# Kernel tuning notes

Hardware: AMD Instinct MI355X
Metric: run time of the kernel (lower is better)

The kernel has to match this reference:

```python
import jax, jax.numpy as jnp
import numpy as np

EPS = 1e-5   # BatchNorm eps (torch default)
K_IMP = 600  # hard-coded k in PointNet.forward


def _bn3(x, g, b, m, v):
    # inference-mode BatchNorm1d over [B, C, N]
    inv = g / jnp.sqrt(v + EPS)
    return (x - m[None, :, None]) * inv[None, :, None] + b[None, :, None]


def _bn2(x, g, b, m, v):
    # inference-mode BatchNorm1d over [B, C]
    inv = g / jnp.sqrt(v + EPS)
    return (x - m[None, :]) * inv[None, :] + b[None, :]


def _full(x, W1, g1, b1, m1, v1, W2, g2, b2, m2, v2, W3, g3, b3, m3, v3,
          W4, g4, b4, m4, v4, W5, g5, b5, m5, v5, L1w, g6, b6, m6, v6, L2w, L2b):
    # pointwise conv1d (k=1) == per-point matmul
    h = jax.nn.relu(_bn3(jnp.einsum('oc,bcn->bon', W1, x), g1, b1, m1, v1))
    h = jax.nn.relu(_bn3(jnp.einsum('oc,bcn->bon', W2, h), g2, b2, m2, v2))
    h = jax.nn.relu(_bn3(jnp.einsum('oc,bcn->bon', W3, h), g3, b3, m3, v3))
    h = jax.nn.relu(_bn3(jnp.einsum('oc,bcn->bon', W4, h), g4, b4, m4, v4))
    feats = jax.nn.relu(_bn3(jnp.einsum('oc,bcn->bon', W5, h), g5, b5, m5, v5))  # [B, emb, N]
    pooled = jnp.max(feats, axis=-1)                       # adaptive_max_pool1d(.,1).squeeze()
    h = jax.nn.relu(_bn2(pooled @ L1w.T, g6, b6, m6, v6))  # dropout is identity in eval
    logits = h @ L2w.T + L2b
    return logits, feats


def reference(x, W1, g1, b1, m1, v1, W2, g2, b2, m2, v2, W3, g3, b3, m3, v3,
              W4, g4, b4, m4, v4, W5, g5, b5, m5, v5, L1w, g6, b6, m6, v6, L2w, L2b):
    P = (W1, g1, b1, m1, v1, W2, g2, b2, m2, v2, W3, g3, b3, m3, v3,
         W4, g4, b4, m4, v4, W5, g5, b5, m5, v5, L1w, g6, b6, m6, v6, L2w, L2b)
    # --- extract_importance: inner model call at full N ---
    _, feats = _full(x, *P)
    B, _, N = x.shape
    imp = jnp.argmax(feats, axis=-1)  # [B, emb] point index maximizing each channel (first-occurrence, matches torch)
    # batched bincount(imp[b], minlength=N) -> [B, N]
    counts = jnp.zeros((B, N), jnp.int32).at[jnp.arange(B)[:, None], imp].add(1)
    idx = jnp.argsort(counts, axis=-1)[:, :K_IMP]          # ascending, take k least-hit bins
    x_sel = jnp.take_along_axis(x, idx[:, None, :], axis=-1)  # gather [B, 3, k]
    # --- main pass on reduced cloud ---
    logits, _ = _full(x_sel, *P)
    return logits


def setup_inputs() -> dict:
    key = jax.random.key(0)
    ks = iter(jax.random.split(key, 64))
    B, N, EMB, NCLS = 16, 8192, 1024, 40

    def randn(shape, s=1.0):
        return jax.random.normal(next(ks), shape, jnp.float32) * s

    inp = {"x": randn((B, 3, N))}
    dims = [(64, 3), (64, 64), (64, 64), (128, 64), (EMB, 128)]
    for i, (o, c) in enumerate(dims, 1):
        inp[f"W{i}"] = randn((o, c), 1.0 / np.sqrt(c))
        inp[f"g{i}"] = 1.0 + randn((o,), 0.1)
        inp[f"b{i}"] = randn((o,), 0.1)
        inp[f"m{i}"] = randn((o,), 0.1)
        inp[f"v{i}"] = jax.random.uniform(next(ks), (o,), jnp.float32, 0.5, 1.5)
    inp["L1w"] = randn((512, EMB), 1.0 / np.sqrt(EMB))
    inp["g6"] = 1.0 + randn((512,), 0.1)
    inp["b6"] = randn((512,), 0.1)
    inp["m6"] = randn((512,), 0.1)
    inp["v6"] = jax.random.uniform(next(ks), (512,), jnp.float32, 0.5, 1.5)
    inp["L2w"] = randn((NCLS, 512), 1.0 / np.sqrt(512))
    inp["L2b"] = randn((NCLS,), 0.01)
    return inp
```

## Files before the change

kernel.cpp:

```cpp
#include <hip/hip_runtime.h>
#include <cstdint>

typedef uint16_t u16;
typedef unsigned int u32;
typedef __attribute__((ext_vector_type(8))) short bf16x8;
typedef __attribute__((ext_vector_type(4))) float f32x4;

union U4V { uint4 u; bf16x8 v; };

#define EPSBN 1e-5f

__device__ __forceinline__ float bf2f(u16 h) {
  return __uint_as_float(((unsigned)h) << 16);
}
__device__ __forceinline__ u16 f2bf(float f) {
  unsigned u = __float_as_uint(f);
  unsigned r = u + 0x7fffu + ((u >> 16) & 1u);
  return (u16)(r >> 16);
}

__global__ void k0_prep(const float* __restrict__ W5,
                        const float* __restrict__ W1, const float* __restrict__ W2,
                        const float* __restrict__ W3, const float* __restrict__ W4,
                        const float* g1, const float* b1, const float* m1, const float* v1,
                        const float* g2, const float* b2, const float* m2, const float* v2,
                        const float* g3, const float* b3, const float* m3, const float* v3,
                        const float* g4, const float* b4, const float* m4, const float* v4,
                        u16* __restrict__ W5h, u16* __restrict__ W5l,
                        u16* __restrict__ W2h, u16* __restrict__ W2l,
                        u16* __restrict__ W3h, u16* __restrict__ W3l,
                        u16* __restrict__ W4h, u16* __restrict__ W4l,
                        float* __restrict__ Wf)
{
  int idx = blockIdx.x * 256 + threadIdx.x;
  if (idx < 131072) {
    int f = idx;
    int j = f & 7, l15 = (f >> 3) & 15, quad = (f >> 7) & 3, ks = (f >> 9) & 3, g = f >> 11;
    float w = W5[(g * 16 + l15) * 128 + ks * 32 + quad * 8 + j];
    u16 hi = f2bf(w);
    W5h[f] = hi;
    W5l[f] = f2bf(w - bf2f(hi));
    return;
  }
  int j = idx - 131072;
  if (j < 16384) {
    const float* src; u16 *dh, *dl; int f;
    if (j < 4096)      { src = W2; dh = W2h; dl = W2l; f = j; }
    else if (j < 8192) { src = W3; dh = W3h; dl = W3l; f = j - 4096; }
    else               { src = W4; dh = W4h; dl = W4l; f = j - 8192; }
    int jj = f & 7;
    int lane = (f >> 3) & 63;
    int t = f >> 9;
    int ks = t & 1, tn = t >> 1;
    int l15 = lane & 15, quad = lane >> 4;
    float w = src[(tn * 16 + l15) * 64 + ks * 32 + quad * 8 + jj];
    u16 hi = f2bf(w);
    dh[f] = hi;
    dl[f] = f2bf(w - bf2f(hi));
  } else if (j < 16576) {
    Wf[j] = W1[j - 16384];
  } else if (j < 16896) {
    int t = j - 16576;
    const float *g, *bb, *mm, *vv; int ch;
    if (t < 64)       { g = g1; bb = b1; mm = m1; vv = v1; ch = t;       }
    else if (t < 128) { g = g2; bb = b2; mm = m2; vv = v2; ch = t - 64;  }
    else if (t < 192) { g = g3; bb = b3; mm = m3; vv = v3; ch = t - 128; }
    else              { g = g4; bb = b4; mm = m4; vv = v4; ch = t - 192; }
    float s = g[ch] / sqrtf(vv[ch] + EPSBN);
    Wf[16576 + t] = s;
    Wf[16896 + t] = bb[ch] - mm[ch] * s;
  }
}

__global__ __launch_bounds__(128, 2) void k1_conv(
    const float* __restrict__ x, const float* __restrict__ Wf,
    const u16* __restrict__ W2h, const u16* __restrict__ W2l,
    const u16* __restrict__ W3h, const u16* __restrict__ W3l,
    const u16* __restrict__ W4h, const u16* __restrict__ W4l,
    u16* __restrict__ H4a, u16* __restrict__ H4b)
{
  __shared__ u32 T[2][64 * 68];
  __shared__ float P1[832];
  const int tid = threadIdx.x;
  const int w = tid >> 6, lane = tid & 63;
  const int l15 = lane & 15, quad = lane >> 4;
  const int base = blockIdx.x * 128 + w * 64;
  const int b = base >> 13, n0 = base & 8191;

  for (int i = tid; i < 832; i += 128)
    P1[i] = (i < 192) ? Wf[16384 + i]
          : (i < 512) ? Wf[16576 + (i - 192)]
                      : Wf[16896 + (i - 512)];
  __syncthreads();
  u32* Tw = &T[w][0];
  const float* SCs = &P1[192];
  const float* SHs = &P1[512];
  const f32x4 vzero = {0.f, 0.f, 0.f, 0.f};

  float xl0 = x[(b * 3 + 0) * 8192 + n0 + lane];
  float xl1 = x[(b * 3 + 1) * 8192 + n0 + lane];
  float xl2 = x[(b * 3 + 2) * 8192 + n0 + lane];
  float xs0[4], xs1[4], xs2[4];
  #pragma unroll
  for (int tm = 0; tm < 4; ++tm) {
    xs0[tm] = __shfl(xl0, tm * 16 + l15, 64);
    xs1[tm] = __shfl(xl1, tm * 16 + l15, 64);
    xs2[tm] = __shfl(xl2, tm * 16 + l15, 64);
  }
  bf16x8 ah[2][4], al[2][4];
  #pragma unroll
  for (int ks = 0; ks < 2; ++ks)
    #pragma unroll
    for (int tm = 0; tm < 4; ++tm) {
      u32 hp[4], lp[4];
      #pragma unroll
      for (int jp = 0; jp < 4; ++jp) {
        u32 hpair = 0, lpair = 0;
        #pragma unroll
        for (int e = 0; e < 2; ++e) {
          int ch = ks * 32 + quad * 8 + jp * 2 + e;
          float c = P1[ch * 3] * xs0[tm];
          c = fmaf(P1[ch * 3 + 1], xs1[tm], c);
          c = fmaf(P1[ch * 3 + 2], xs2[tm], c);
          float v = fmaxf(0.f, fmaf(c, SCs[ch], SHs[ch]));
          u16 hi = f2bf(v); float er = v - bf2f(hi); u16 lo = f2bf(er);
          hpair |= ((u32)hi) << (16 * e);
          lpair |= ((u32)lo) << (16 * e);
        }
        hp[jp] = hpair; lp[jp] = lpair;
      }
      U4V th, tl;
      th.u.x = hp[0]; th.u.y = hp[1]; th.u.z = hp[2]; th.u.w = hp[3];
      tl.u.x = lp[0]; tl.u.y = lp[1]; tl.u.z = lp[2]; tl.u.w = lp[3];
      ah[ks][tm] = th.v; al[ks][tm] = tl.v;
    }

  {
    f32x4 acc[4][4];
    #pragma unroll
    for (int tm = 0; tm < 4; ++tm)
      #pragma unroll
      for (int tn = 0; tn < 4; ++tn) acc[tm][tn] = vzero;
    #pragma unroll
    for (int ks = 0; ks < 2; ++ks) {
      bf16x8 bh[4], bl[4];
      #pragma unroll
      for (int tn = 0; tn < 4; ++tn) {
        int idx = ((tn * 2 + ks) * 64 + lane) * 8;
        bh[tn] = *(const bf16x8*)&W2h[idx];
        bl[tn] = *(const bf16x8*)&W2l[idx];
      }
      #pragma unroll
      for (int tm = 0; tm < 4; ++tm)
        #pragma unroll
        for (int tn = 0; tn < 4; ++tn) {
          acc[tm][tn] = __builtin_amdgcn_mfma_f32_16x16x32_bf16(ah[ks][tm], bh[tn], acc[tm][tn], 0, 0, 0);
          acc[tm][tn] = __builtin_amdgcn_mfma_f32_16x16x32_bf16(ah[ks][tm], bl[tn], acc[tm][tn], 0, 0, 0);
          acc[tm][tn] = __builtin_amdgcn_mfma_f32_16x16x32_bf16(al[ks][tm], bh[tn], acc[tm][tn], 0, 0, 0);
        }
    }
    #pragma unroll
    for (int tn = 0; tn < 4; ++tn) {
      int ch = tn * 16 + l15;
      float sc = SCs[64 + ch], sh = SHs[64 + ch];
      #pragma unroll
      for (int tm = 0; tm < 4; ++tm)
        #pragma unroll
        for (int r = 0; r < 4; ++r) {
          float v = fmaxf(0.f, fmaf(acc[tm][tn][r], sc, sh));
          u16 hi = f2bf(v); float er = v - bf2f(hi); u16 lo = f2bf(er);
          Tw[(tm * 16 + quad * 4 + r) * 68 + ch] = (u32)hi | ((u32)lo << 16);
        }
    }
  }

  #pragma unroll
  for (int ks = 0; ks < 2; ++ks)
    #pragma unroll
    for (int tm = 0; tm < 4; ++tm) {
      const uint4 p0 = *(const uint4*)&Tw[(tm * 16 + l15) * 68 + ks * 32 + quad * 8];
      const uint4 p1 = *(const uint4*)&Tw[(tm * 16 + l15) * 68 + ks * 32 + quad * 8 + 4];
      U4V th, tl;
      th.u.x = (p0.x & 0xffffu) | (p0.y << 16);
      th.u.y = (p0.z & 0xffffu) | (p0.w << 16);
      th.u.z = (p1.x & 0xffffu) | (p1.y << 16);
      th.u.w = (p1.z & 0xffffu) | (p1.w << 16);
      tl.u.x = (p0.x >> 16) | (p0.y & 0xffff0000u);
      tl.u.y = (p0.z >> 16) | (p0.w & 0xffff0000u);
      tl.u.z = (p1.x >> 16) | (p1.y & 0xffff0000u);
      tl.u.w = (p1.z >> 16) | (p1.w & 0xffff0000u);
      ah[ks][tm] = th.v; al[ks][tm] = tl.v;
    }
  {
    f32x4 acc[4][4];
    #pragma unroll
    for (int tm = 0; tm < 4; ++tm)
      #pragma unroll
      for (int tn = 0; tn < 4; ++tn) acc[tm][tn] = vzero;
    #pragma unroll
    for (int ks = 0; ks < 2; ++ks) {
      bf16x8 bh[4], bl[4];
      #pragma unroll
      for (int tn = 0; tn < 4; ++tn) {
        int idx = ((tn * 2 + ks) * 64 + lane) * 8;
        bh[tn] = *(const bf16x8*)&W3h[idx];
        bl[tn] = *(const bf16x8*)&W3l[idx];
      }
      #pragma unroll
      for (int tm = 0; tm < 4; ++tm)
        #pragma unroll
        for (int tn = 0; tn < 4; ++tn) {
          acc[tm][tn] = __builtin_amdgcn_mfma_f32_16x16x32_bf16(ah[ks][tm], bh[tn], acc[tm][tn], 0, 0, 0);
          acc[tm][tn] = __builtin_amdgcn_mfma_f32_16x16x32_bf16(ah[ks][tm], bl[tn], acc[tm][tn], 0, 0, 0);
          acc[tm][tn] = __builtin_amdgcn_mfma_f32_16x16x32_bf16(al[ks][tm], bh[tn], acc[tm][tn], 0, 0, 0);
        }
    }
    #pragma unroll
    for (int tn = 0; tn < 4; ++tn) {
      int ch = tn * 16 + l15;
      float sc = SCs[128 + ch], sh = SHs[128 + ch];
      #pragma unroll
      for (int tm = 0; tm < 4; ++tm)
        #pragma unroll
        for (int r = 0; r < 4; ++r) {
          float v = fmaxf(0.f, fmaf(acc[tm][tn][r], sc, sh));
          u16 hi = f2bf(v); float er = v - bf2f(hi); u16 lo = f2bf(er);
          Tw[(tm * 16 + quad * 4 + r) * 68 + ch] = (u32)hi | ((u32)lo << 16);
        }
    }
  }

  #pragma unroll
  for (int ks = 0; ks < 2; ++ks)
    #pragma unroll
    for (int tm = 0; tm < 4; ++tm) {
      const uint4 p0 = *(const uint4*)&Tw[(tm * 16 + l15) * 68 + ks * 32 + quad * 8];
      const uint4 p1 = *(const uint4*)&Tw[(tm * 16 + l15) * 68 + ks * 32 + quad * 8 + 4];
      U4V th, tl;
      th.u.x = (p0.x & 0xffffu) | (p0.y << 16);
      th.u.y = (p0.z & 0xffffu) | (p0.w << 16);
      th.u.z = (p1.x & 0xffffu) | (p1.y << 16);
      th.u.w = (p1.z & 0xffffu) | (p1.w << 16);
      tl.u.x = (p0.x >> 16) | (p0.y & 0xffff0000u);
      tl.u.y = (p0.z >> 16) | (p0.w & 0xffff0000u);
      tl.u.z = (p1.x >> 16) | (p1.y & 0xffff0000u);
      tl.u.w = (p1.z >> 16) | (p1.w & 0xffff0000u);
      ah[ks][tm] = th.v; al[ks][tm] = tl.v;
    }
  for (int half = 0; half < 2; ++half) {
    f32x4 acc[4][4];
    #pragma unroll
    for (int tm = 0; tm < 4; ++tm)
      #pragma unroll
      for (int tn = 0; tn < 4; ++tn) acc[tm][tn] = vzero;
    #pragma unroll
    for (int ks = 0; ks < 2; ++ks) {
      bf16x8 bh[4], bl[4];
      #pragma unroll
      for (int tn = 0; tn < 4; ++tn) {
        int idx = (((half * 4 + tn) * 2 + ks) * 64 + lane) * 8;
        bh[tn] = *(const bf16x8*)&W4h[idx];
        bl[tn] = *(const bf16x8*)&W4l[idx];
      }
      #pragma unroll
      for (int tm = 0; tm < 4; ++tm)
        #pragma unroll
        for (int tn = 0; tn < 4; ++tn) {
          acc[tm][tn] = __builtin_amdgcn_mfma_f32_16x16x32_bf16(ah[ks][tm], bh[tn], acc[tm][tn], 0, 0, 0);
          acc[tm][tn] = __builtin_amdgcn_mfma_f32_16x16x32_bf16(ah[ks][tm], bl[tn], acc[tm][tn], 0, 0, 0);
          acc[tm][tn] = __builtin_amdgcn_mfma_f32_16x16x32_bf16(al[ks][tm], bh[tn], acc[tm][tn], 0, 0, 0);
        }
    }
    #pragma unroll
    for (int tn = 0; tn < 4; ++tn) {
      int ch = half * 64 + tn * 16 + l15;
      float sc = SCs[192 + ch], sh = SHs[192 + ch];
      #pragma unroll
      for (int tm = 0; tm < 4; ++tm)
        #pragma unroll
        for (int r = 0; r < 4; ++r) {
          float v = fmaxf(0.f, fmaf(acc[tm][tn][r], sc, sh));
          u16 hi = f2bf(v); float er = v - bf2f(hi); u16 lo = f2bf(er);
          Tw[(tm * 16 + quad * 4 + r) * 68 + tn * 16 + l15] = (u32)hi | ((u32)lo << 16);
        }
    }
    #pragma unroll
    for (int kg = 0; kg < 8; ++kg) {
      const uint4 p0 = *(const uint4*)&Tw[lane * 68 + kg * 8];
      const uint4 p1 = *(const uint4*)&Tw[lane * 68 + kg * 8 + 4];
      uint4 hu, lu;
      hu.x = (p0.x & 0xffffu) | (p0.y << 16);
      hu.y = (p0.z & 0xffffu) | (p0.w << 16);
      hu.z = (p1.x & 0xffffu) | (p1.y << 16);
      hu.w = (p1.z & 0xffffu) | (p1.w << 16);
      lu.x = (p0.x >> 16) | (p0.y & 0xffff0000u);
      lu.y = (p0.z >> 16) | (p0.w & 0xffff0000u);
      lu.z = (p1.x >> 16) | (p1.y & 0xffff0000u);
      lu.w = (p1.z >> 16) | (p1.w & 0xffff0000u);
      size_t e = ((size_t)(b * 16 + half * 8 + kg) * 8192 + n0 + lane) * 8;
      *(uint4*)&H4a[e] = hu;
      *(uint4*)&H4b[e] = lu;
    }
  }
}

__global__ __launch_bounds__(256, 2) void k2_gemm(
    const u16* __restrict__ H4a, const u16* __restrict__ H4b,
    const u16* __restrict__ W5h, const u16* __restrict__ W5l,
    const int* __restrict__ sel,
    int P, int PS, int TPB,
    float* __restrict__ pmax, int* __restrict__ pidx)
{
  __shared__ u16 Ah[16 * 512];
  __shared__ u16 Al[16 * 512];

  const int blk = blockIdx.x;
  const int nc = (blk >> 3) & 3;
  const int p  = ((blk >> 5) << 3) + (blk & 7);
  const int b  = p / PS;
  const int ps = p % PS;
  const int tid = threadIdx.x;
  const int lane = tid & 63, wv = tid >> 6;
  const int l15 = lane & 15, quad = lane >> 4;

  bf16x8 bh[4][4];
  #pragma unroll
  for (int ks = 0; ks < 4; ++ks)
    #pragma unroll
    for (int tn = 0; tn < 4; ++tn) {
      int g = nc * 16 + wv * 4 + tn;
      bh[ks][tn] = *(const bf16x8*)&W5h[(size_t)(g * 4 + ks) * 512 + lane * 8];
    }

  float runM[4]; int runI[4];
  #pragma unroll
  for (int tn = 0; tn < 4; ++tn) { runM[tn] = -3.4e38f; runI[tn] = 0x7FFFFFFF; }

  const f32x4 vzero = {0.f, 0.f, 0.f, 0.f};

  for (int t = 0; t < TPB; ++t) {
    const int mb = (ps * TPB + t) << 6;
    if (mb >= P) break;

    __syncthreads();
    #pragma unroll
    for (int i = 0; i < 4; ++i) {
      int c = i * 4 + wv;
      uint4 va; va.x = va.y = va.z = va.w = 0u;
      uint4 vb; vb.x = vb.y = vb.z = vb.w = 0u;
      if (sel) {
        int pt = mb + lane;
        if (pt < P) {
          int n0 = sel[b * 600 + pt] & 8191;
          size_t e = ((size_t)(b * 16 + c) * 8192 + n0) * 8;
          va = *(const uint4*)&H4a[e];
          vb = *(const uint4*)&H4b[e];
        }
      } else {
        size_t e = ((size_t)(b * 16 + c) * 8192 + (mb + lane)) * 8;
        va = *(const uint4*)&H4a[e];
        vb = *(const uint4*)&H4b[e];
      }
      *(uint4*)&Ah[c * 512 + lane * 8] = va;
      *(uint4*)&Al[c * 512 + lane * 8] = vb;
    }
    __syncthreads();

    f32x4 acc[4][4];
    #pragma unroll
    for (int tm = 0; tm < 4; ++tm)
      #pragma unroll
      for (int tn = 0; tn < 4; ++tn)
        acc[tm][tn] = vzero;

    #pragma unroll
    for (int ks = 0; ks < 4; ++ks) {
      bf16x8 bl[4], afh[4], afl[4];
      #pragma unroll
      for (int tn = 0; tn < 4; ++tn) {
        int g = nc * 16 + wv * 4 + tn;
        bl[tn] = *(const bf16x8*)&W5l[(size_t)(g * 4 + ks) * 512 + lane * 8];
      }
      #pragma unroll
      for (int tm = 0; tm < 4; ++tm) {
        int off = (ks * 4 + quad) * 512 + (tm * 16 + l15) * 8;
        afh[tm] = *(const bf16x8*)&Ah[off];
        afl[tm] = *(const bf16x8*)&Al[off];
      }
      #pragma unroll
      for (int tm = 0; tm < 4; ++tm)
        #pragma unroll
        for (int tn = 0; tn < 4; ++tn) {
          acc[tm][tn] = __builtin_amdgcn_mfma_f32_16x16x32_bf16(afh[tm], bh[ks][tn], acc[tm][tn], 0, 0, 0);
          acc[tm][tn] = __builtin_amdgcn_mfma_f32_16x16x32_bf16(afh[tm], bl[tn],     acc[tm][tn], 0, 0, 0);
          acc[tm][tn] = __builtin_amdgcn_mfma_f32_16x16x32_bf16(afl[tm], bh[ks][tn], acc[tm][tn], 0, 0, 0);
        }
    }

    #pragma unroll
    for (int tn = 0; tn < 4; ++tn) {
      #pragma unroll
      for (int tm = 0; tm < 4; ++tm) {
        #pragma unroll
        for (int r = 0; r < 4; ++r) {
          int pt = mb + tm * 16 + (quad << 2) + r;
          float v = acc[tm][tn][r];
          if (pt < P && v > runM[tn]) { runM[tn] = v; runI[tn] = pt; }
        }
      }
    }
  }

  #pragma unroll
  for (int tn = 0; tn < 4; ++tn) {
    float rM = runM[tn]; int rI = runI[tn];
    #pragma unroll
    for (int mk = 16; mk <= 32; mk <<= 1) {
      float v2 = __shfl_xor(rM, mk, 64);
      int   i2 = __shfl_xor(rI, mk, 64);
      if (v2 > rM || (v2 == rM && i2 < rI)) { rM = v2; rI = i2; }
    }
    if (quad == 0) {
      int ch = nc * 256 + wv * 64 + tn * 16 + l15;
      size_t o = ((size_t)b * 1024 + ch) * (size_t)PS + ps;
      pmax[o] = rM; pidx[o] = rI;
    }
  }
}

__global__ __launch_bounds__(256) void k3_select(
    const float* __restrict__ pmax, const int* __restrict__ pidx, int PS,
    const float* __restrict__ g5, const float* __restrict__ b5,
    const float* __restrict__ m5, const float* __restrict__ v5,
    int* __restrict__ sel)
{
  __shared__ unsigned char used[8192];
  __shared__ int cnts[256];
  __shared__ int pref[256];
  const int b = blockIdx.x, tid = threadIdx.x;

  #pragma unroll
  for (int i = 0; i < 8; ++i) ((int*)used)[i * 256 + tid] = 0;
  __syncthreads();

  for (int ch = tid; ch < 1024; ch += 256) {
    const float* pm = pmax + (((size_t)b << 10) + ch) * PS;
    const int*   pi = pidx + (((size_t)b << 10) + ch) * PS;
    float bm = pm[0]; int bi = pi[0];
    for (int s2 = 1; s2 < PS; ++s2) {
      float v = pm[s2]; int ii = pi[s2];
      if (v > bm || (v == bm && ii < bi)) { bm = v; bi = ii; }
    }
    float s5 = g5[ch] / sqrtf(v5[ch] + EPSBN);
    float z = fmaf(bm, s5, b5[ch] - m5[ch] * s5);
    int idx = (z > 0.f) ? (bi & 8191) : 0;
    used[idx] = 1;
  }
  __syncthreads();

  const int base = tid << 5;
  int c = 0;
  #pragma unroll
  for (int i = 0; i < 32; ++i) c += (used[base + i] == 0) ? 1 : 0;
  cnts[tid] = c;
  __syncthreads();
  if (tid == 0) {
    int r = 0;
    for (int i = 0; i < 256; ++i) { pref[i] = r; r += cnts[i]; }
  }
  __syncthreads();
  int rank = pref[tid];
  for (int i = 0; i < 32; ++i) {
    int n0 = base + i;
    if (!used[n0]) { if (rank < 600) sel[b * 600 + rank] = n0; ++rank; }
  }
}

__global__ __launch_bounds__(256) void k6a_fc1(
    const float* __restrict__ pmax2, int PS2,
    const float* __restrict__ g5, const float* __restrict__ b5,
    const float* __restrict__ m5, const float* __restrict__ v5,
    const float* __restrict__ L1w,
    const float* __restrict__ g6, const float* __restrict__ b6,
    const float* __restrict__ m6, const float* __restrict__ v6,
    float* __restrict__ h6buf)
{
  __shared__ float pooled[1024];
  __shared__ float part[128][2];
  const int b = blockIdx.x >> 2, rc = blockIdx.x & 3;
  const int tid = threadIdx.x;

  for (int ch = tid; ch < 1024; ch += 256) {
    const float* pm = pmax2 + (((size_t)b << 10) + ch) * PS2;
    float raw = pm[0];
    for (int s2 = 1; s2 < PS2; ++s2) raw = fmaxf(raw, pm[s2]);
    float s5 = g5[ch] / sqrtf(v5[ch] + EPSBN);
    pooled[ch] = fmaxf(0.f, fmaf(raw, s5, b5[ch] - m5[ch] * s5));
  }
  __syncthreads();

  const int rl = tid & 127;
  const int hf = tid >> 7;
  const int o  = rc * 128 + rl;
  float a0 = 0.f, a1 = 0.f, a2 = 0.f, a3 = 0.f;
  const int j0 = hf * 512;
  for (int j = j0; j < j0 + 512; j += 8) {
    float4 w0 = *(const float4*)&L1w[(size_t)o * 1024 + j];
    float4 w1 = *(const float4*)&L1w[(size_t)o * 1024 + j + 4];
    float4 p0 = *(const float4*)&pooled[j];
    float4 p1 = *(const float4*)&pooled[j + 4];
    a0 = fmaf(w0.x, p0.x, a0); a1 = fmaf(w0.y, p0.y, a1);
    a2 = fmaf(w0.z, p0.z, a2); a3 = fmaf(w0.w, p0.w, a3);
    a0 = fmaf(w1.x, p1.x, a0); a1 = fmaf(w1.y, p1.y, a1);
    a2 = fmaf(w1.z, p1.z, a2); a3 = fmaf(w1.w, p1.w, a3);
  }
  part[rl][hf] = (a0 + a1) + (a2 + a3);
  __syncthreads();

  if (tid < 128) {
    int oo = rc * 128 + tid;
    float acc = part[tid][0] + part[tid][1];
    float s6 = g6[oo] / sqrtf(v6[oo] + EPSBN);
    h6buf[b * 512 + oo] = fmaxf(0.f, fmaf(acc, s6, b6[oo] - m6[oo] * s6));
  }
}

__global__ __launch_bounds__(64) void k6b_fc2(
    const float* __restrict__ h6buf,
    const float* __restrict__ L2w, const float* __restrict__ L2b,
    float* __restrict__ out)
{
  const int b = blockIdx.x, tid = threadIdx.x;
  if (tid < 40) {
    const float* h6 = h6buf + b * 512;
    float acc = L2b[tid];
    for (int j = 0; j < 512; j += 4) {
      float4 wv = *(const float4*)&L2w[(size_t)tid * 512 + j];
      float4 hv = *(const float4*)&h6[j];
      acc = fmaf(wv.x, hv.x, acc);
      acc = fmaf(wv.y, hv.y, acc);
      acc = fmaf(wv.z, hv.z, acc);
      acc = fmaf(wv.w, hv.w, acc);
    }
    out[b * 40 + tid] = acc;
  }
}

extern "C" void kernel_launch(void* const* d_in, const int* in_sizes, int n_in,
                              void* d_out, int out_size, void* d_ws, size_t ws_size,
                              hipStream_t stream)
{
  (void)in_sizes; (void)n_in; (void)out_size; (void)ws_size;
  const float* x   = (const float*)d_in[0];
  const float* W1  = (const float*)d_in[1];
  const float* g1  = (const float*)d_in[2];
  const float* b1  = (const float*)d_in[3];
  const float* m1  = (const float*)d_in[4];
  const float* v1  = (const float*)d_in[5];
  const float* W2  = (const float*)d_in[6];
  const float* g2  = (const float*)d_in[7];
  const float* b2  = (const float*)d_in[8];
  const float* m2  = (const float*)d_in[9];
  const float* v2  = (const float*)d_in[10];
  const float* W3  = (const float*)d_in[11];
  const float* g3  = (const float*)d_in[12];
  const float* b3  = (const float*)d_in[13];
  const float* m3  = (const float*)d_in[14];
  const float* v3  = (const float*)d_in[15];
  const float* W4  = (const float*)d_in[16];
  const float* g4  = (const float*)d_in[17];
  const float* b4  = (const float*)d_in[18];
  const float* m4  = (const float*)d_in[19];
  const float* v4  = (const float*)d_in[20];
  const float* W5  = (const float*)d_in[21];
  const float* g5  = (const float*)d_in[22];
  const float* b5  = (const float*)d_in[23];
  const float* m5  = (const float*)d_in[24];
  const float* v5  = (const float*)d_in[25];
  const float* L1w = (const float*)d_in[26];
  const float* g6  = (const float*)d_in[27];
  const float* b6  = (const float*)d_in[28];
  const float* m6  = (const float*)d_in[29];
  const float* v6  = (const float*)d_in[30];
  const float* L2w = (const float*)d_in[31];
  const float* L2b = (const float*)d_in[32];

  char* ws = (char*)d_ws;
  float* Wf    = (float*)(ws + 0);
  u16*   W5h   = (u16*)(ws + 69632);
  u16*   W5l   = (u16*)(ws + 331776);
  u16*   W2h   = (u16*)(ws + 593920);
  u16*   W2l   = (u16*)(ws + 602112);
  u16*   W3h   = (u16*)(ws + 610304);
  u16*   W3l   = (u16*)(ws + 618496);
  u16*   W4h   = (u16*)(ws + 626688);
  u16*   W4l   = (u16*)(ws + 643072);
  u16*   H4a   = (u16*)(ws + 659456);
  u16*   H4b   = (u16*)(ws + 34213888);
  float* pmax  = (float*)(ws + 67768320);
  int*   pidx  = (int*)(ws + 68816896);
  float* pmax2 = (float*)(ws + 69865472);
  int*   pidx2 = (int*)(ws + 70520832);
  int*   sel   = (int*)(ws + 71176192);
  float* h6buf = (float*)(ws + 71215104);

  k0_prep<<<578, 256, 0, stream>>>(W5, W1, W2, W3, W4,
                                   g1, b1, m1, v1, g2, b2, m2, v2,
                                   g3, b3, m3, v3, g4, b4, m4, v4,
                                   W5h, W5l, W2h, W2l, W3h, W3l, W4h, W4l, Wf);
  k1_conv<<<1024, 128, 0, stream>>>(x, Wf, W2h, W2l, W3h, W3l, W4h, W4l,
                                    H4a, H4b);
  k2_gemm<<<1024, 256, 0, stream>>>(H4a, H4b, W5h, W5l, nullptr,
                                    8192, 16, 8, pmax, pidx);
  k3_select<<<16, 256, 0, stream>>>(pmax, pidx, 16, g5, b5, m5, v5, sel);
  k2_gemm<<<640, 256, 0, stream>>>(H4a, H4b, W5h, W5l, sel,
                                   600, 10, 1, pmax2, pidx2);
  k6a_fc1<<<64, 256, 0, stream>>>(pmax2, 10, g5, b5, m5, v5, L1w,
                                  g6, b6, m6, v6, h6buf);
  k6b_fc2<<<16, 64, 0, stream>>>(h6buf, L2w, L2b, (float*)d_out);
}
```

Before: 309.0 us.

## Add specialized full-cloud W5 GEMM keeping W5 high half in registers

Adds a dedicated kernel for the full-N layer-5 GEMM plus argmax pass, replacing the generic k2_gemm for that call. The new kernel preloads the W5 high-half fragments into registers once per block and streams two 64-point A tiles per iteration through a larger shared buffer, with the per-channel running max/argmax fused into the epilogue. It aims to cut repeated weight loads and sync count, at the cost of higher register and LDS pressure, which may lower occupancy.

```diff
diff --git a/kernel.cpp b/kernel.cpp
--- a/kernel.cpp
+++ b/kernel.cpp
@@ -300,6 +300,131 @@
       size_t e = ((size_t)(b * 16 + half * 8 + kg) * 8192 + n0 + lane) * 8;
       *(uint4*)&H4a[e] = hu;
       *(uint4*)&H4b[e] = lu;
+    }
+  }
+}
+
+__global__ __launch_bounds__(256, 2) void k2a_gemm(
+    const u16* __restrict__ H4a, const u16* __restrict__ H4b,
+    const u16* __restrict__ W5h, const u16* __restrict__ W5l,
+    float* __restrict__ pmax, int* __restrict__ pidx)
+{
+  __shared__ u16 AA[2][2][16 * 512];
+
+  const int blk = blockIdx.x;
+  const int nc = (blk >> 3) & 3;
+  const int p  = ((blk >> 5) << 3) + (blk & 7);
+  const int b  = p >> 4;
+  const int ps = p & 15;
+  const int tid = threadIdx.x;
+  const int lane = tid & 63, wv = tid >> 6;
+  const int l15 = lane & 15, quad = lane >> 4;
+
+  bf16x8 bh[4][4];
+  #pragma unroll
+  for (int ks = 0; ks < 4; ++ks)
+    #pragma unroll
+    for (int tn = 0; tn < 4; ++tn) {
+      int g = nc * 16 + wv * 4 + tn;
+      bh[ks][tn] = *(const bf16x8*)&W5h[(size_t)(g * 4 + ks) * 512 + lane * 8];
+    }
+
+  const u16* pa[4];
+  const u16* pb[4];
+  #pragma unroll
+  for (int i = 0; i < 4; ++i) {
+    int c = i * 4 + wv;
+    size_t e = ((size_t)(b * 16 + c) * 8192 + ps * 512 + lane) * 8;
+    pa[i] = H4a + e;
+    pb[i] = H4b + e;
+  }
+
+  float runM[4]; int runI[4];
+  #pragma unroll
+  for (int tn = 0; tn < 4; ++tn) { runM[tn] = -3.4e38f; runI[tn] = 0; }
+
+  const f32x4 vzero = {0.f, 0.f, 0.f, 0.f};
+
+  for (int tp = 0; tp < 4; ++tp) {
+    __syncthreads();
+    #pragma unroll
+    for (int u = 0; u < 2; ++u) {
+      #pragma unroll
+      for (int i = 0; i < 4; ++i) {
+        int c = i * 4 + wv;
+        uint4 va = *(const uint4*)(pa[i] + u * 512);
+        uint4 vb = *(const uint4*)(pb[i] + u * 512);
+        *(uint4*)&AA[u][0][c * 512 + lane * 8] = va;
+        *(uint4*)&AA[u][1][c * 512 + lane * 8] = vb;
+      }
+    }
+    __syncthreads();
+
+    #pragma unroll
+    for (int u = 0; u < 2; ++u) {
+      const int mb = ps * 512 + tp * 128 + u * 64;
+      f32x4 acc[4][4];
+      #pragma unroll
+      for (int tm = 0; tm < 4; ++tm)
+        #pragma unroll
+        for (int tn = 0; tn < 4; ++tn)
+          acc[tm][tn] = vzero;
+
+      #pragma unroll
+      for (int ks = 0; ks < 4; ++ks) {
+        bf16x8 bl[4], afh[4], afl[4];
+        #pragma unroll
+        for (int tn = 0; tn < 4; ++tn) {
+          int g = nc * 16 + wv * 4 + tn;
+          bl[tn] = *(const bf16x8*)&W5l[(size_t)(g * 4 + ks) * 512 + lane * 8];
+        }
+        #pragma unroll
+        for (int tm = 0; tm < 4; ++tm) {
+          int off = (ks * 4 + quad) * 512 + (tm * 16 + l15) * 8;
+          afh[tm] = *(const bf16x8*)&AA[u][0][off];
+          afl[tm] = *(const bf16x8*)&AA[u][1][off];
+        }
+        #pragma unroll
+        for (int tm = 0; tm < 4; ++tm)
+          #pragma unroll
+          for (int tn = 0; tn < 4; ++tn) {
+            acc[tm][tn] = __builtin_amdgcn_mfma_f32_16x16x32_bf16(afh[tm], bh[ks][tn], acc[tm][tn], 0, 0, 0);
+            acc[tm][tn] = __builtin_amdgcn_mfma_f32_16x16x32_bf16(afh[tm], bl[tn],     acc[tm][tn], 0, 0, 0);
+            acc[tm][tn] = __builtin_amdgcn_mfma_f32_16x16x32_bf16(afl[tm], bh[ks][tn], acc[tm][tn], 0, 0, 0);
+          }
+      }
+
+      #pragma unroll
+      for (int tn = 0; tn < 4; ++tn) {
+        #pragma unroll
+        for (int tm = 0; tm < 4; ++tm) {
+          #pragma unroll
+          for (int r = 0; r < 4; ++r) {
+            int pt = mb + tm * 16 + (quad << 2) + r;
+            float v = acc[tm][tn][r];
+            if (v > runM[tn]) { runM[tn] = v; runI[tn] = pt; }
+          }
+        }
+      }
+    }
+
+    #pragma unroll
+    for (int i = 0; i < 4; ++i) { pa[i] += 1024; pb[i] += 1024; }
+  }
+
+  #pragma unroll
+  for (int tn = 0; tn < 4; ++tn) {
+    float rM = runM[tn]; int rI = runI[tn];
+    #pragma unroll
+    for (int mk = 16; mk <= 32; mk <<= 1) {
+      float v2 = __shfl_xor(rM, mk, 64);
+      int   i2 = __shfl_xor(rI, mk, 64);
+      if (v2 > rM || (v2 == rM && i2 < rI)) { rM = v2; rI = i2; }
+    }
+    if (quad == 0) {
+      int ch = nc * 256 + wv * 64 + tn * 16 + l15;
+      size_t o = (((size_t)b * 1024 + ch) << 4) + ps;
+      pmax[o] = rM; pidx[o] = rI;
     }
   }
 }
@@ -610,8 +735,7 @@
                                    W5h, W5l, W2h, W2l, W3h, W3l, W4h, W4l, Wf);
   k1_conv<<<1024, 128, 0, stream>>>(x, Wf, W2h, W2l, W3h, W3l, W4h, W4l,
                                     H4a, H4b);
-  k2_gemm<<<1024, 256, 0, stream>>>(H4a, H4b, W5h, W5l, nullptr,
-                                    8192, 16, 8, pmax, pidx);
+  k2a_gemm<<<1024, 256, 0, stream>>>(H4a, H4b, W5h, W5l, pmax, pidx);
   k3_select<<<16, 256, 0, stream>>>(pmax, pidx, 16, g5, b5, m5, v5, sel);
   k2_gemm<<<640, 256, 0, stream>>>(H4a, H4b, W5h, W5l, sel,
                                    600, 10, 1, pmax2, pidx2);
```

New measurement: 294.0 us. 4.9% less time.
